# Performance work log

Measured on AMD Instinct MI355X. Metric: run time of the kernel, lower is better.

## Reference

```python
import jax, jax.numpy as jnp
import numpy as np

N = 50000   # nodes
E = 800000  # edges
D = 128     # hidden_dim
O = 128     # out_dim (must equal hidden_dim; see prior_mean Linear)
T = 16      # number of timesteps for the modeled time encoding
EPS = 1e-9


def _gcn(x, W, b, src, dst, ew, n):
    """PyG-style GCNConv: add self-loops, symmetric deg^-1/2 normalization."""
    loop = jnp.arange(n)
    s = jnp.concatenate([src, loop])
    d = jnp.concatenate([dst, loop])
    w = jnp.concatenate([ew, jnp.ones((n,), x.dtype)])
    deg = jax.ops.segment_sum(w, d, num_segments=n)
    dinv = jnp.where(deg > 0, jax.lax.rsqrt(deg), 0.0)
    norm = dinv[s] * w * dinv[d]              # [E+N]
    h = x @ W                                  # [N, out]
    out = jax.ops.segment_sum(h[s] * norm[:, None], d, num_segments=n)
    return out + b


def setup_inputs() -> dict:
    key = jax.random.key(0)
    ks = jax.random.split(key, 20)

    def lin(k, fan_in, fan_out):
        return jax.random.normal(k, (fan_in, fan_out), jnp.float32) / np.sqrt(fan_in)

    return {
        "edge_index": jax.random.randint(ks[0], (2, E), 0, N, dtype=jnp.int64),
        "x": jax.random.normal(ks[1], (N, D), jnp.float32),
        "t": 3,
        "edge_score": jax.random.uniform(ks[2], (E,), jnp.float32),
        "total_len": 16,
        "train_len": 12,
        "W_enc": lin(ks[3], D, D), "b_enc": jnp.zeros((D,), jnp.float32),
        "W_mu": lin(ks[4], D, O), "b_mu": jnp.zeros((O,), jnp.float32),
        "W_std": lin(ks[5], D, O), "b_std": jnp.zeros((O,), jnp.float32),
        "W_prior": lin(ks[6], D, O), "b_prior": jnp.zeros((O,), jnp.float32),
        "W_pm": lin(ks[7], D, O), "b_pm": jnp.zeros((O,), jnp.float32),
        "W_ps": lin(ks[8], D, O), "b_ps": jnp.zeros((O,), jnp.float32),
        "time_emb": 0.02 * jax.random.normal(ks[9], (T, O), jnp.float32),
    }


def reference(edge_index, x, t, edge_score, total_len, train_len,
              W_enc, b_enc, W_mu, b_mu, W_std, b_std,
              W_prior, b_prior, W_pm, b_pm, W_ps, b_ps, time_emb):
    src, dst = edge_index[0], edge_index[1]
    n = x.shape[0]
    ones_e = jnp.ones((src.shape[0],), x.dtype)

    # encoder
    enc_t = jax.nn.relu(_gcn(x, W_enc, b_enc, src, dst, edge_score, n))
    # drop = 0.0 -> dropout is identity
    enc_mean_t = _gcn(enc_t, W_mu, b_mu, src, dst, ones_e, n)
    enc_std_t = jax.nn.sigmoid(_gcn(enc_t, W_std, b_std, src, dst, ones_e, n))

    # reparameterize (fixed eps for determinism)
    eps = jax.random.normal(jax.random.key(42), enc_mean_t.shape, enc_mean_t.dtype)
    conf_z_t = eps * enc_std_t + enc_mean_t

    # prior branch: time_encoding(prior, t) modeled as additive time embedding
    prior = jax.nn.relu(_gcn(x, W_prior, b_prior, src, dst, ones_e, n))
    prior = prior + time_emb[t]
    prior_mean = prior @ W_pm + b_pm
    prior_std = jax.nn.sigmoid(prior @ W_ps + b_ps)

    # fused KL divergence
    kl = (2.0 * jnp.log(prior_std + EPS) - 2.0 * jnp.log(enc_std_t + EPS)
          + ((enc_std_t + EPS) ** 2 + (enc_mean_t - prior_mean) ** 2)
          / (prior_std + EPS) ** 2 - 1.0)
    kl_loss = 0.5 * jnp.mean(jnp.sum(kl, axis=1), axis=0)
    return kl_loss, conf_z_t
```

## Files before the change

kernel.cpp:

```cpp
#include <hip/hip_runtime.h>
#include <math.h>

#define D 128

typedef unsigned int u32;
typedef unsigned short u16;
typedef __attribute__((ext_vector_type(8))) short bf16x8;
typedef __attribute__((ext_vector_type(4))) float f32x4;
typedef __attribute__((ext_vector_type(4))) u32 u32x4;

__device__ __forceinline__ u32 rotl32(u32 x, int r){ return (x<<r) | (x>>(32-r)); }

__device__ __forceinline__ u16 f2bf(float x){
  u32 u = __float_as_uint(x);
  return (u16)((u + 0x7fffu + ((u >> 16) & 1u)) >> 16);
}
__device__ __forceinline__ float bf2f(u16 h){ return __uint_as_float(((u32)h) << 16); }

__device__ __forceinline__ float jax_normal_part_xor(u32 m){
  const u32 ks0 = 0u, ks1 = 42u, ks2 = 0x1BD11BF0u;
  u32 x0 = 0u + ks0;
  u32 x1 = m  + ks1;
  #define TF_R4(a,b,c,d) \
    x0 += x1; x1 = rotl32(x1,(a)); x1 ^= x0; \
    x0 += x1; x1 = rotl32(x1,(b)); x1 ^= x0; \
    x0 += x1; x1 = rotl32(x1,(c)); x1 ^= x0; \
    x0 += x1; x1 = rotl32(x1,(d)); x1 ^= x0;
  TF_R4(13,15,26,6)   x0 += ks1; x1 += ks2 + 1u;
  TF_R4(17,29,16,24)  x0 += ks2; x1 += ks0 + 2u;
  TF_R4(13,15,26,6)   x0 += ks0; x1 += ks1 + 3u;
  TF_R4(17,29,16,24)  x0 += ks1; x1 += ks2 + 4u;
  TF_R4(13,15,26,6)   x0 += ks2; x1 += ks0 + 5u;
  #undef TF_R4
  u32 bits = x0 ^ x1;
  float f = __uint_as_float((bits >> 9) | 0x3F800000u) - 1.0f;
  const float LO = -0.99999994f;
  float u = fmaxf(LO, f * 2.0f + LO);
  float w = -__logf(fmaf(-u, u, 1.0f));
  float p;
  if (w < 5.0f){
    w -= 2.5f;
    p =  2.81022636e-08f;
    p = fmaf(p, w,  3.43273939e-07f);
    p = fmaf(p, w, -3.5233877e-06f);
    p = fmaf(p, w, -4.39150654e-06f);
    p = fmaf(p, w,  0.00021858087f);
    p = fmaf(p, w, -0.00125372503f);
    p = fmaf(p, w, -0.00417768164f);
    p = fmaf(p, w,  0.246640727f);
    p = fmaf(p, w,  1.50140941f);
  } else {
    w = sqrtf(w) - 3.0f;
    p = -0.000200214257f;
    p = fmaf(p, w,  0.000100950558f);
    p = fmaf(p, w,  0.00134934322f);
    p = fmaf(p, w, -0.00367342844f);
    p = fmaf(p, w,  0.00573950773f);
    p = fmaf(p, w, -0.0076224613f);
    p = fmaf(p, w,  0.00943887047f);
    p = fmaf(p, w,  1.00167406f);
    p = fmaf(p, w,  2.83297682f);
  }
  return 1.41421354f * (p * u);
}

__device__ __forceinline__ float sigmoidf_(float z){ return 1.0f / (1.0f + __expf(-z)); }

__global__ __launch_bounds__(256) void k_eps(u32* __restrict__ epsb, int half_total){
  int idx = blockIdx.x*256 + threadIdx.x;
  int stride = gridDim.x*256;
  for (int i = idx; i < half_total; i += stride){
    u32 m0 = 2u*(u32)i;
    float e0 = jax_normal_part_xor(m0);
    float e1 = jax_normal_part_xor(m0 + 1u);
    epsb[i] = (u32)f2bf(e0) | ((u32)f2bf(e1) << 16);
  }
}

__global__ void k_detect(const u32* __restrict__ e_u32, int* __restrict__ flag){
  __shared__ int s_nz;
  if (threadIdx.x == 0) s_nz = 0;
  __syncthreads();
  if (e_u32[2*threadIdx.x + 1] != 0u) atomicAdd(&s_nz, 1);
  __syncthreads();
  if (threadIdx.x == 0) *flag = (s_nz == 0) ? 1 : 0;
}

__global__ void k_norm(const void* __restrict__ eidx, const int* __restrict__ flag,
                       int* __restrict__ src_w, int* __restrict__ dst_w, int e){
  int i = blockIdx.x*256 + threadIdx.x;
  if (i >= e) return;
  if (*flag){
    const u32* u = (const u32*)eidx;
    src_w[i] = (int)u[2*(size_t)i];
    dst_w[i] = (int)u[2*((size_t)e + i)];
  } else {
    const int* p = (const int*)eidx;
    src_w[i] = p[i];
    dst_w[i] = p[e + i];
  }
}

__global__ void k_init(int* __restrict__ cnt, int n){
  int i = blockIdx.x*256 + threadIdx.x;
  if (i < n) cnt[i] = 0;
}

__global__ void k_hist(const int* __restrict__ dst, int* __restrict__ cnt, int e){
  int i = blockIdx.x*256 + threadIdx.x;
  if (i >= e) return;
  atomicAdd(&cnt[dst[i]], 1);
}

__global__ __launch_bounds__(256) void k_scan1(const int* __restrict__ cnt,
                                               int* __restrict__ rp,
                                               int* __restrict__ bsum, int n){
  __shared__ int sh[256];
  int tid = threadIdx.x, idx = blockIdx.x*256 + tid;
  int v = (idx < n) ? cnt[idx] : 0;
  sh[tid] = v; __syncthreads();
  for (int off = 1; off < 256; off <<= 1){
    int t = (tid >= off) ? sh[tid-off] : 0;
    __syncthreads(); sh[tid] += t; __syncthreads();
  }
  if (idx < n) rp[idx] = sh[tid] - v;
  if (tid == 255) bsum[blockIdx.x] = sh[255];
}

__global__ __launch_bounds__(1024) void k_scan2(int* __restrict__ bsum, int nb){
  __shared__ int sh[1024];
  int tid = threadIdx.x;
  int v = (tid < nb) ? bsum[tid] : 0;
  sh[tid] = v; __syncthreads();
  for (int off = 1; off < 1024; off <<= 1){
    int t = (tid >= off) ? sh[tid-off] : 0;
    __syncthreads(); sh[tid] += t; __syncthreads();
  }
  if (tid < nb) bsum[tid] = sh[tid] - v;
}

__global__ void k_scan3(int* __restrict__ rp, int* __restrict__ cur,
                        const int* __restrict__ bsum, const int* __restrict__ cnt,
                        float* __restrict__ dinv_o, int n, int e){
  int idx = blockIdx.x*256 + threadIdx.x;
  if (idx < n){
    int r = rp[idx] + bsum[blockIdx.x];
    rp[idx] = r; cur[idx] = r;
    dinv_o[idx] = rsqrtf((float)(cnt[idx] + 1));
  }
  if (idx == 0) rp[n] = e;
}

__global__ void k_scatter(const int* __restrict__ src, const int* __restrict__ dst,
                          const float* __restrict__ sc, int* __restrict__ cur,
                          int* __restrict__ col, float* __restrict__ wsrt, int e){
  int i = blockIdx.x*256 + threadIdx.x;
  if (i >= e) return;
  int d = dst[i];
  int p = atomicAdd(&cur[d], 1);
  col[p] = src[i];
  wsrt[p] = sc[i];
}

__global__ void k_deg(const int* __restrict__ rp, const float* __restrict__ wsrt,
                      float* __restrict__ dinv_s, int n){
  int i = blockIdx.x*256 + threadIdx.x;
  if (i >= n) return;
  float s = 1.0f;
  int e0 = rp[i], e1 = rp[i+1];
  for (int j = e0; j < e1; ++j) s += wsrt[j];
  dinv_s[i] = rsqrtf(s);
}

__global__ void k_wconv(const float* __restrict__ W0, const float* __restrict__ W1,
                        const float* __restrict__ W2, const float* __restrict__ W3,
                        const float* __restrict__ W4, const float* __restrict__ W5,
                        u16* __restrict__ wt){
  const float* Ws[6] = {W0,W1,W2,W3,W4,W5};
  const float* W = Ws[blockIdx.y];
  u16* Wt = wt + (size_t)blockIdx.y*16384;
  int idx = blockIdx.x*256 + threadIdx.x;
  int k = idx >> 7, col = idx & 127;
  Wt[col*128 + k] = f2bf(W[idx]);
}

__global__ __launch_bounds__(256) void k_agg_dual(
    const float* __restrict__ x, const int* __restrict__ rp,
    const int* __restrict__ col, const float* __restrict__ wsrt,
    const float* __restrict__ dinv_s, const float* __restrict__ dinv_o,
    u16* __restrict__ out_s, u16* __restrict__ out_o, int n){
  int wid = (blockIdx.x * 256 + threadIdx.x) >> 6;
  int lane = threadIdx.x & 63;
  if (wid >= n) return;
  const float2* x2 = (const float2*)x;
  float dsv = dinv_s[wid], dov = dinv_o[wid];
  float2 xv = x2[(size_t)wid*64 + lane];
  float ss = dsv*dsv, oo = dov*dov;
  float2 as = { xv.x*ss, xv.y*ss };
  float2 ao = { xv.x*oo, xv.y*oo };
  int e0 = rp[wid], e1 = rp[wid+1];
  for (int base = e0; base < e1; base += 64){
    int cnt = e1 - base; if (cnt > 64) cnt = 64;
    int idx = base + (lane < cnt ? lane : cnt - 1);
    int   sl = col[idx];
    float wl = wsrt[idx];
    float nsl = dinv_s[sl] * wl * dsv;
    float nol = dinv_o[sl] * dov;
    int j = 0;
    for (; j + 4 <= cnt; j += 4){
      int   s0=__shfl(sl,j),   s1=__shfl(sl,j+1),   s2=__shfl(sl,j+2),   s3=__shfl(sl,j+3);
      float a0=__shfl(nsl,j),  a1=__shfl(nsl,j+1),  a2=__shfl(nsl,j+2),  a3=__shfl(nsl,j+3);
      float b0=__shfl(nol,j),  b1=__shfl(nol,j+1),  b2=__shfl(nol,j+2),  b3=__shfl(nol,j+3);
      float2 r0 = x2[(size_t)s0*64 + lane];
      float2 r1 = x2[(size_t)s1*64 + lane];
      float2 r2 = x2[(size_t)s2*64 + lane];
      float2 r3 = x2[(size_t)s3*64 + lane];
      as.x = fmaf(a0,r0.x,as.x); as.y = fmaf(a0,r0.y,as.y);
      ao.x = fmaf(b0,r0.x,ao.x); ao.y = fmaf(b0,r0.y,ao.y);
      as.x = fmaf(a1,r1.x,as.x); as.y = fmaf(a1,r1.y,as.y);
      ao.x = fmaf(b1,r1.x,ao.x); ao.y = fmaf(b1,r1.y,ao.y);
      as.x = fmaf(a2,r2.x,as.x); as.y = fmaf(a2,r2.y,as.y);
      ao.x = fmaf(b2,r2.x,ao.x); ao.y = fmaf(b2,r2.y,ao.y);
      as.x = fmaf(a3,r3.x,as.x); as.y = fmaf(a3,r3.y,as.y);
      ao.x = fmaf(b3,r3.x,ao.x); ao.y = fmaf(b3,r3.y,ao.y);
    }
    for (; j < cnt; ++j){
      int   s0=__shfl(sl,j);
      float a0=__shfl(nsl,j), b0=__shfl(nol,j);
      float2 r0 = x2[(size_t)s0*64 + lane];
      as.x = fmaf(a0,r0.x,as.x); as.y = fmaf(a0,r0.y,as.y);
      ao.x = fmaf(b0,r0.x,ao.x); ao.y = fmaf(b0,r0.y,ao.y);
    }
  }
  ((u32*)out_s)[(size_t)wid*64 + lane] = (u32)f2bf(as.x) | ((u32)f2bf(as.y) << 16);
  ((u32*)out_o)[(size_t)wid*64 + lane] = (u32)f2bf(ao.x) | ((u32)f2bf(ao.y) << 16);
}

__global__ __launch_bounds__(256) void k_agg_one(
    const u16* __restrict__ h, const int* __restrict__ rp,
    const int* __restrict__ col, const float* __restrict__ dinv_o,
    u16* __restrict__ out, int n){
  int wid = (blockIdx.x * 256 + threadIdx.x) >> 6;
  int lane = threadIdx.x & 63;
  if (wid >= n) return;
  const u32* h2 = (const u32*)h;
  float dov = dinv_o[wid];
  u32 hv = h2[(size_t)wid*64 + lane];
  float oo = dov*dov;
  float2 ao = { bf2f((u16)(hv & 0xffff))*oo, bf2f((u16)(hv >> 16))*oo };
  int e0 = rp[wid], e1 = rp[wid+1];
  for (int base = e0; base < e1; base += 64){
    int cnt = e1 - base; if (cnt > 64) cnt = 64;
    int idx = base + (lane < cnt ? lane : cnt - 1);
    int   sl = col[idx];
    float nol = dinv_o[sl] * dov;
    int j = 0;
    for (; j + 4 <= cnt; j += 4){
      int   s0=__shfl(sl,j),  s1=__shfl(sl,j+1),  s2=__shfl(sl,j+2),  s3=__shfl(sl,j+3);
      float b0=__shfl(nol,j), b1=__shfl(nol,j+1), b2=__shfl(nol,j+2), b3=__shfl(nol,j+3);
      u32 r0 = h2[(size_t)s0*64 + lane];
      u32 r1 = h2[(size_t)s1*64 + lane];
      u32 r2 = h2[(size_t)s2*64 + lane];
      u32 r3 = h2[(size_t)s3*64 + lane];
      ao.x = fmaf(b0, bf2f((u16)(r0&0xffff)), ao.x); ao.y = fmaf(b0, bf2f((u16)(r0>>16)), ao.y);
      ao.x = fmaf(b1, bf2f((u16)(r1&0xffff)), ao.x); ao.y = fmaf(b1, bf2f((u16)(r1>>16)), ao.y);
      ao.x = fmaf(b2, bf2f((u16)(r2&0xffff)), ao.x); ao.y = fmaf(b2, bf2f((u16)(r2>>16)), ao.y);
      ao.x = fmaf(b3, bf2f((u16)(r3&0xffff)), ao.x); ao.y = fmaf(b3, bf2f((u16)(r3>>16)), ao.y);
    }
    for (; j < cnt; ++j){
      int   s0=__shfl(sl,j);
      float b0=__shfl(nol,j);
      u32 r0 = h2[(size_t)s0*64 + lane];
      ao.x = fmaf(b0, bf2f((u16)(r0&0xffff)), ao.x); ao.y = fmaf(b0, bf2f((u16)(r0>>16)), ao.y);
    }
  }
  ((u32*)out)[(size_t)wid*64 + lane] = (u32)f2bf(ao.x) | ((u32)f2bf(ao.y) << 16);
}


__global__ __launch_bounds__(256) void k_mfma_act2(
    const u16* __restrict__ A0, const u16* __restrict__ Wt0, const float* __restrict__ b0,
    const u16* __restrict__ A1, const u16* __restrict__ Wt1, const float* __restrict__ b1,
    const float* __restrict__ temb, const int* __restrict__ t_ptr,
    u16* __restrict__ out0, u16* __restrict__ out1, int n){
  const int sl = blockIdx.y;
  const u16* A  = sl ? A1 : A0;
  const u16* Wt = sl ? Wt1 : Wt0;
  const float* b = sl ? b1 : b0;
  u16* out = sl ? out1 : out0;
  const int tid = threadIdx.x;
  const int lane = tid & 63, wave = tid >> 6;
  const int lr = lane & 15, lg = lane >> 4;
  const int rw = wave >> 1, cw = wave & 1;
  const int row0 = blockIdx.x*32 + rw*16;
  int rowf = row0 + lr;
  int rowc = rowf < n ? rowf : n - 1;
  const char* Arow = (const char*)A + (size_t)rowc*256;
  const char* Wb   = (const char*)Wt + (cw*64 + lr)*256 + lg*16;
  f32x4 z = {0.f,0.f,0.f,0.f};
  f32x4 acc[4];
  #pragma unroll
  for (int i = 0; i < 4; ++i) acc[i] = z;
  #pragma unroll
  for (int ks = 0; ks < 4; ++ks){
    bf16x8 a = *(const bf16x8*)(Arow + ks*64 + lg*16);
    #pragma unroll
    for (int cf = 0; cf < 4; ++cf){
      bf16x8 bb = *(const bf16x8*)(Wb + cf*16*256 + ks*64);
      acc[cf] = __builtin_amdgcn_mfma_f32_16x16x32_bf16(a, bb, acc[cf], 0, 0, 0);
    }
  }
  int t = sl ? *t_ptr : 0;
  int rbase = row0 + (lg << 2);
  #pragma unroll
  for (int cf = 0; cf < 4; ++cf){
    int colw = cw*64 + cf*16 + lr;
    float bb = b[colw];
    float tt = sl ? temb[t*128 + colw] : 0.f;
    #pragma unroll
    for (int r = 0; r < 4; ++r){
      int row = rbase + r;
      if (row < n)
        out[(size_t)row*128 + colw] = f2bf(fmaxf(acc[cf][r] + bb, 0.f) + tt);
    }
  }
}

__global__ __launch_bounds__(256) void k_mfma_quad(
    const u16* __restrict__ Apr, const u16* __restrict__ Aen,
    const u16* __restrict__ Wtpm, const float* __restrict__ bpm,
    const u16* __restrict__ Wtps, const float* __restrict__ bps,
    const u16* __restrict__ Wtmu, const float* __restrict__ bmu,
    const u16* __restrict__ Wtsd, const float* __restrict__ bsd,
    const u32* __restrict__ epsb,
    float* __restrict__ conf, float* __restrict__ pblk, int n){
  const int tid = threadIdx.x;
  const int lane = tid & 63, wave = tid >> 6;
  const int lr = lane & 15, lg = lane >> 4;
  const int rw = wave >> 1, cw = wave & 1;
  const int row0 = blockIdx.x*32 + rw*16;
  int rowf = row0 + lr;
  int rowc = rowf < n ? rowf : n - 1;
  const char* Ap = (const char*)Apr + (size_t)rowc*256;
  const char* Ae = (const char*)Aen + (size_t)rowc*256;
  const int wcb = (cw*64 + lr)*256 + lg*16;
  const char* Wpm = (const char*)Wtpm + wcb;
  const char* Wps = (const char*)Wtps + wcb;
  const char* Wmu = (const char*)Wtmu + wcb;
  const char* Wsd = (const char*)Wtsd + wcb;
  f32x4 z = {0.f,0.f,0.f,0.f};
  f32x4 aPM[4], aPS[4], aMU[4], aSD[4];
  #pragma unroll
  for (int i = 0; i < 4; ++i){ aPM[i]=z; aPS[i]=z; aMU[i]=z; aSD[i]=z; }
  #pragma unroll
  for (int ks = 0; ks < 4; ++ks){
    bf16x8 a5 = *(const bf16x8*)(Ap + ks*64 + lg*16);
    bf16x8 a2 = *(const bf16x8*)(Ae + ks*64 + lg*16);
    #pragma unroll
    for (int cf = 0; cf < 4; ++cf){
      int off = cf*16*256 + ks*64;
      aPM[cf] = __builtin_amdgcn_mfma_f32_16x16x32_bf16(a5, *(const bf16x8*)(Wpm+off), aPM[cf], 0,0,0);
      aPS[cf] = __builtin_amdgcn_mfma_f32_16x16x32_bf16(a5, *(const bf16x8*)(Wps+off), aPS[cf], 0,0,0);
      aMU[cf] = __builtin_amdgcn_mfma_f32_16x16x32_bf16(a2, *(const bf16x8*)(Wmu+off), aMU[cf], 0,0,0);
      aSD[cf] = __builtin_amdgcn_mfma_f32_16x16x32_bf16(a2, *(const bf16x8*)(Wsd+off), aSD[cf], 0,0,0);
    }
  }
  const float EPS = 1e-9f;
  int rbase = row0 + (lg << 2);
  float klsum = 0.f;
  #pragma unroll
  for (int cf = 0; cf < 4; ++cf){
    int colw = cw*64 + cf*16 + lr;
    float bb1 = bpm[colw], bb2 = bps[colw];
    float bb3 = bmu[colw], bb4 = bsd[colw];
    #pragma unroll
    for (int r = 0; r < 4; ++r){
      int row = rbase + r;
      if (row < n){
        size_t m = (size_t)row*128 + colw;
        float pmv = aPM[cf][r] + bb1;
        float psv = sigmoidf_(aPS[cf][r] + bb2);
        float em  = aMU[cf][r] + bb3;
        float es  = sigmoidf_(aSD[cf][r] + bb4);
        u32 ew = epsb[m >> 1];
        float eps = bf2f((u16)((colw & 1) ? (ew >> 16) : (ew & 0xffff)));
        conf[m] = fmaf(eps, es, em);
        float es_e = es + EPS, ps_e = psv + EPS;
        float diff = em - pmv;
        klsum += 2.0f*__logf(ps_e/es_e)
               + (es_e*es_e + diff*diff) / (ps_e*ps_e) - 1.0f;
      }
    }
  }
  #pragma unroll
  for (int off = 32; off > 0; off >>= 1) klsum += __shfl_down(klsum, off);
  __shared__ float wsum[4];
  if ((tid & 63) == 0) wsum[tid >> 6] = klsum;
  __syncthreads();
  if (tid == 0) pblk[blockIdx.x] = wsum[0] + wsum[1] + wsum[2] + wsum[3];
}

__global__ __launch_bounds__(256) void k_finish(const float* __restrict__ pblk, int nb,
                                                float* __restrict__ out0, int n){
  __shared__ double sh[256];
  double s = 0.0;
  for (int i = threadIdx.x; i < nb; i += 256) s += (double)pblk[i];
  sh[threadIdx.x] = s; __syncthreads();
  for (int off = 128; off > 0; off >>= 1){
    if (threadIdx.x < off) sh[threadIdx.x] += sh[threadIdx.x + off];
    __syncthreads();
  }
  if (threadIdx.x == 0) out0[0] = (float)(0.5 * sh[0] / (double)n);
}

extern "C" void kernel_launch(void* const* d_in, const int* in_sizes, int n_in,
                              void* d_out, int out_size, void* d_ws, size_t ws_size,
                              hipStream_t stream){
  const void*  eidx   = d_in[0];
  const float* x      = (const float*)d_in[1];
  const int*   t_ptr  = (const int*)d_in[2];
  const float* escore = (const float*)d_in[3];
  const float* W_enc = (const float*)d_in[6];  const float* b_enc = (const float*)d_in[7];
  const float* W_mu  = (const float*)d_in[8];  const float* b_mu  = (const float*)d_in[9];
  const float* W_std = (const float*)d_in[10]; const float* b_std = (const float*)d_in[11];
  const float* W_pr  = (const float*)d_in[12]; const float* b_pr  = (const float*)d_in[13];
  const float* W_pm  = (const float*)d_in[14]; const float* b_pm  = (const float*)d_in[15];
  const float* W_ps  = (const float*)d_in[16]; const float* b_ps  = (const float*)d_in[17];
  const float* temb  = (const float*)d_in[18];

  const int N = in_sizes[1] / D;
  const int E = in_sizes[3];

  char* w = (char*)d_ws;
  auto alloc = [&](size_t bytes) -> char* {
    char* p = w; w += (bytes + 255) & ~(size_t)255; return p;
  };
  int*    flag   = (int*)   alloc(256);
  int*    src_w  = (int*)   alloc((size_t)E*4);
  int*    dst_w  = (int*)   alloc((size_t)E*4);
  int*    cnt    = (int*)   alloc((size_t)N*4);
  int*    rp     = (int*)   alloc((size_t)(N+1)*4);
  int*    cur    = (int*)   alloc((size_t)N*4);
  float*  dinv_s = (float*) alloc((size_t)N*4);
  float*  dinv_o = (float*) alloc((size_t)N*4);
  int*    bsum   = (int*)   alloc(1024*4);
  int*    col    = (int*)   alloc((size_t)E*4);
  float*  wsrt   = (float*) alloc((size_t)E*4);
  u16*    wt     = (u16*)   alloc((size_t)6*16384*2);
  u16*    B1     = (u16*)   alloc((size_t)N*D*2);
  u16*    B2     = (u16*)   alloc((size_t)N*D*2);
  u16*    B3     = (u16*)   alloc((size_t)N*D*2);
  u16*    B5     = (u16*)   alloc((size_t)N*D*2);
  u32*    EPSB   = (u32*)   alloc((size_t)N*64*4);
  const int gG32 = (N + 31) / 32;
  float*  pblk   = (float*) alloc((size_t)gG32*4);
  (void)ws_size; (void)n_in; (void)out_size;

  float* conf = ((float*)d_out) + 1;

  u16* Wt_enc = wt + 0*16384;
  u16* Wt_pr  = wt + 1*16384;
  u16* Wt_pm  = wt + 2*16384;
  u16* Wt_ps  = wt + 3*16384;
  u16* Wt_mu  = wt + 4*16384;
  u16* Wt_std = wt + 5*16384;

  const int gE  = (E + 255) / 256;
  const int gN  = (N + 255) / 256;
  const int gW  = (N * 64 + 255) / 256;

  k_eps    <<<2048, 256, 0, stream>>>(EPSB, N*64);
  k_wconv  <<<dim3(64,6), 256, 0, stream>>>(W_enc, W_pr, W_pm, W_ps, W_mu, W_std, wt);
  k_detect <<<1, 256, 0, stream>>>((const u32*)eidx, flag);
  k_norm   <<<gE, 256, 0, stream>>>(eidx, flag, src_w, dst_w, E);
  k_init   <<<gN, 256, 0, stream>>>(cnt, N);
  k_hist   <<<gE, 256, 0, stream>>>(dst_w, cnt, E);
  k_scan1  <<<gN, 256, 0, stream>>>(cnt, rp, bsum, N);
  k_scan2  <<<1, 1024, 0, stream>>>(bsum, gN);
  k_scan3  <<<gN, 256, 0, stream>>>(rp, cur, bsum, cnt, dinv_o, N, E);
  k_scatter<<<gE, 256, 0, stream>>>(src_w, dst_w, escore, cur, col, wsrt, E);
  k_deg    <<<gN, 256, 0, stream>>>(rp, wsrt, dinv_s, N);

  k_agg_dual<<<gW, 256, 0, stream>>>(x, rp, col, wsrt, dinv_s, dinv_o, B1, B2, N);
  k_mfma_act2<<<dim3(gG32,2), 256, 0, stream>>>(B1, Wt_enc, b_enc, B2, Wt_pr, b_pr,
                                                temb, t_ptr, B3, B5, N);
  k_agg_one<<<gW, 256, 0, stream>>>(B3, rp, col, dinv_o, B2, N);
  k_mfma_quad<<<gG32, 256, 0, stream>>>(B5, B2, Wt_pm, b_pm, Wt_ps, b_ps,
                                        Wt_mu, b_mu, Wt_std, b_std, EPSB,
                                        conf, pblk, N);
  k_finish<<<1, 256, 0, stream>>>(pblk, gG32, (float*)d_out, N);
}
```

Measured before the change: 337.7 us.

## Fuse neighbor aggregation into MFMA GEMM kernels via LDS staging

Merges each sparse aggregation pass with the dense GEMM that follows it. Each 32-row block gathers its neighbor sums into swizzled shared memory, then runs the MFMA tiles from LDS, which removes the bf16 intermediate buffers B1/B2 and two launches. The edge histogram is also folded into the edge-index normalization kernel. In exchange, each block now runs a serial 8-rows-per-wave gather before its MFMA phase, and the grid drops to N/32 blocks, which lowers parallelism for the latency-bound gather.

```diff
diff --git a/kernel.cpp b/kernel.cpp
--- a/kernel.cpp
+++ b/kernel.cpp
@@ -7,7 +7,6 @@
 typedef unsigned short u16;
 typedef __attribute__((ext_vector_type(8))) short bf16x8;
 typedef __attribute__((ext_vector_type(4))) float f32x4;
-typedef __attribute__((ext_vector_type(4))) u32 u32x4;
 
 __device__ __forceinline__ u32 rotl32(u32 x, int r){ return (x<<r) | (x>>(32-r)); }
 
@@ -86,30 +85,29 @@
   if (threadIdx.x == 0) *flag = (s_nz == 0) ? 1 : 0;
 }
 
-__global__ void k_norm(const void* __restrict__ eidx, const int* __restrict__ flag,
-                       int* __restrict__ src_w, int* __restrict__ dst_w, int e){
-  int i = blockIdx.x*256 + threadIdx.x;
-  if (i >= e) return;
-  if (*flag){
-    const u32* u = (const u32*)eidx;
-    src_w[i] = (int)u[2*(size_t)i];
-    dst_w[i] = (int)u[2*((size_t)e + i)];
-  } else {
-    const int* p = (const int*)eidx;
-    src_w[i] = p[i];
-    dst_w[i] = p[e + i];
-  }
-}
-
 __global__ void k_init(int* __restrict__ cnt, int n){
   int i = blockIdx.x*256 + threadIdx.x;
   if (i < n) cnt[i] = 0;
 }
 
-__global__ void k_hist(const int* __restrict__ dst, int* __restrict__ cnt, int e){
+__global__ void k_norm(const void* __restrict__ eidx, const int* __restrict__ flag,
+                       int* __restrict__ src_w, int* __restrict__ dst_w,
+                       int* __restrict__ cnt, int e){
   int i = blockIdx.x*256 + threadIdx.x;
   if (i >= e) return;
-  atomicAdd(&cnt[dst[i]], 1);
+  int s, d;
+  if (*flag){
+    const u32* u = (const u32*)eidx;
+    s = (int)u[2*(size_t)i];
+    d = (int)u[2*((size_t)e + i)];
+  } else {
+    const int* p = (const int*)eidx;
+    s = p[i];
+    d = p[e + i];
+  }
+  src_w[i] = s;
+  dst_w[i] = d;
+  atomicAdd(&cnt[d], 1);
 }
 
 __global__ __launch_bounds__(256) void k_scan1(const int* __restrict__ cnt,
@@ -184,165 +182,173 @@
   Wt[col*128 + k] = f2bf(W[idx]);
 }
 
-__global__ __launch_bounds__(256) void k_agg_dual(
+
+__global__ __launch_bounds__(256) void k_fuse1(
     const float* __restrict__ x, const int* __restrict__ rp,
     const int* __restrict__ col, const float* __restrict__ wsrt,
     const float* __restrict__ dinv_s, const float* __restrict__ dinv_o,
-    u16* __restrict__ out_s, u16* __restrict__ out_o, int n){
-  int wid = (blockIdx.x * 256 + threadIdx.x) >> 6;
-  int lane = threadIdx.x & 63;
-  if (wid >= n) return;
-  const float2* x2 = (const float2*)x;
-  float dsv = dinv_s[wid], dov = dinv_o[wid];
-  float2 xv = x2[(size_t)wid*64 + lane];
-  float ss = dsv*dsv, oo = dov*dov;
-  float2 as = { xv.x*ss, xv.y*ss };
-  float2 ao = { xv.x*oo, xv.y*oo };
-  int e0 = rp[wid], e1 = rp[wid+1];
-  for (int base = e0; base < e1; base += 64){
-    int cnt = e1 - base; if (cnt > 64) cnt = 64;
-    int idx = base + (lane < cnt ? lane : cnt - 1);
-    int   sl = col[idx];
-    float wl = wsrt[idx];
-    float nsl = dinv_s[sl] * wl * dsv;
-    float nol = dinv_o[sl] * dov;
-    int j = 0;
-    for (; j + 4 <= cnt; j += 4){
-      int   s0=__shfl(sl,j),   s1=__shfl(sl,j+1),   s2=__shfl(sl,j+2),   s3=__shfl(sl,j+3);
-      float a0=__shfl(nsl,j),  a1=__shfl(nsl,j+1),  a2=__shfl(nsl,j+2),  a3=__shfl(nsl,j+3);
-      float b0=__shfl(nol,j),  b1=__shfl(nol,j+1),  b2=__shfl(nol,j+2),  b3=__shfl(nol,j+3);
-      float2 r0 = x2[(size_t)s0*64 + lane];
-      float2 r1 = x2[(size_t)s1*64 + lane];
-      float2 r2 = x2[(size_t)s2*64 + lane];
-      float2 r3 = x2[(size_t)s3*64 + lane];
-      as.x = fmaf(a0,r0.x,as.x); as.y = fmaf(a0,r0.y,as.y);
-      ao.x = fmaf(b0,r0.x,ao.x); ao.y = fmaf(b0,r0.y,ao.y);
-      as.x = fmaf(a1,r1.x,as.x); as.y = fmaf(a1,r1.y,as.y);
-      ao.x = fmaf(b1,r1.x,ao.x); ao.y = fmaf(b1,r1.y,ao.y);
-      as.x = fmaf(a2,r2.x,as.x); as.y = fmaf(a2,r2.y,as.y);
-      ao.x = fmaf(b2,r2.x,ao.x); ao.y = fmaf(b2,r2.y,ao.y);
-      as.x = fmaf(a3,r3.x,as.x); as.y = fmaf(a3,r3.y,as.y);
-      ao.x = fmaf(b3,r3.x,ao.x); ao.y = fmaf(b3,r3.y,ao.y);
-    }
-    for (; j < cnt; ++j){
-      int   s0=__shfl(sl,j);
-      float a0=__shfl(nsl,j), b0=__shfl(nol,j);
-      float2 r0 = x2[(size_t)s0*64 + lane];
-      as.x = fmaf(a0,r0.x,as.x); as.y = fmaf(a0,r0.y,as.y);
-      ao.x = fmaf(b0,r0.x,ao.x); ao.y = fmaf(b0,r0.y,ao.y);
-    }
-  }
-  ((u32*)out_s)[(size_t)wid*64 + lane] = (u32)f2bf(as.x) | ((u32)f2bf(as.y) << 16);
-  ((u32*)out_o)[(size_t)wid*64 + lane] = (u32)f2bf(ao.x) | ((u32)f2bf(ao.y) << 16);
-}
-
-__global__ __launch_bounds__(256) void k_agg_one(
-    const u16* __restrict__ h, const int* __restrict__ rp,
-    const int* __restrict__ col, const float* __restrict__ dinv_o,
-    u16* __restrict__ out, int n){
-  int wid = (blockIdx.x * 256 + threadIdx.x) >> 6;
-  int lane = threadIdx.x & 63;
-  if (wid >= n) return;
-  const u32* h2 = (const u32*)h;
-  float dov = dinv_o[wid];
-  u32 hv = h2[(size_t)wid*64 + lane];
-  float oo = dov*dov;
-  float2 ao = { bf2f((u16)(hv & 0xffff))*oo, bf2f((u16)(hv >> 16))*oo };
-  int e0 = rp[wid], e1 = rp[wid+1];
-  for (int base = e0; base < e1; base += 64){
-    int cnt = e1 - base; if (cnt > 64) cnt = 64;
-    int idx = base + (lane < cnt ? lane : cnt - 1);
-    int   sl = col[idx];
-    float nol = dinv_o[sl] * dov;
-    int j = 0;
-    for (; j + 4 <= cnt; j += 4){
-      int   s0=__shfl(sl,j),  s1=__shfl(sl,j+1),  s2=__shfl(sl,j+2),  s3=__shfl(sl,j+3);
-      float b0=__shfl(nol,j), b1=__shfl(nol,j+1), b2=__shfl(nol,j+2), b3=__shfl(nol,j+3);
-      u32 r0 = h2[(size_t)s0*64 + lane];
-      u32 r1 = h2[(size_t)s1*64 + lane];
-      u32 r2 = h2[(size_t)s2*64 + lane];
-      u32 r3 = h2[(size_t)s3*64 + lane];
-      ao.x = fmaf(b0, bf2f((u16)(r0&0xffff)), ao.x); ao.y = fmaf(b0, bf2f((u16)(r0>>16)), ao.y);
-      ao.x = fmaf(b1, bf2f((u16)(r1&0xffff)), ao.x); ao.y = fmaf(b1, bf2f((u16)(r1>>16)), ao.y);
-      ao.x = fmaf(b2, bf2f((u16)(r2&0xffff)), ao.x); ao.y = fmaf(b2, bf2f((u16)(r2>>16)), ao.y);
-      ao.x = fmaf(b3, bf2f((u16)(r3&0xffff)), ao.x); ao.y = fmaf(b3, bf2f((u16)(r3>>16)), ao.y);
-    }
-    for (; j < cnt; ++j){
-      int   s0=__shfl(sl,j);
-      float b0=__shfl(nol,j);
-      u32 r0 = h2[(size_t)s0*64 + lane];
-      ao.x = fmaf(b0, bf2f((u16)(r0&0xffff)), ao.x); ao.y = fmaf(b0, bf2f((u16)(r0>>16)), ao.y);
-    }
-  }
-  ((u32*)out)[(size_t)wid*64 + lane] = (u32)f2bf(ao.x) | ((u32)f2bf(ao.y) << 16);
-}
-
-
-__global__ __launch_bounds__(256) void k_mfma_act2(
-    const u16* __restrict__ A0, const u16* __restrict__ Wt0, const float* __restrict__ b0,
-    const u16* __restrict__ A1, const u16* __restrict__ Wt1, const float* __restrict__ b1,
+    const u16* __restrict__ Wt_enc, const float* __restrict__ b_enc,
+    const u16* __restrict__ Wt_pr, const float* __restrict__ b_pr,
     const float* __restrict__ temb, const int* __restrict__ t_ptr,
-    u16* __restrict__ out0, u16* __restrict__ out1, int n){
-  const int sl = blockIdx.y;
-  const u16* A  = sl ? A1 : A0;
-  const u16* Wt = sl ? Wt1 : Wt0;
-  const float* b = sl ? b1 : b0;
-  u16* out = sl ? out1 : out0;
+    u16* __restrict__ enc_out, u16* __restrict__ pri_out, int n){
+  __shared__ u32 A1[32*64];
+  __shared__ u32 A2[32*64];
   const int tid = threadIdx.x;
   const int lane = tid & 63, wave = tid >> 6;
+  const int row0 = blockIdx.x * 32;
+  const float2* x2 = (const float2*)x;
+  for (int i = 0; i < 8; ++i){
+    int row = wave*8 + i;
+    int wid = row0 + row;
+    float2 as = {0.f,0.f}, ao = {0.f,0.f};
+    if (wid < n){
+      float dsv = dinv_s[wid], dov = dinv_o[wid];
+      float2 xv = x2[(size_t)wid*64 + lane];
+      float ss = dsv*dsv, oo = dov*dov;
+      as.x = xv.x*ss; as.y = xv.y*ss;
+      ao.x = xv.x*oo; ao.y = xv.y*oo;
+      int e0 = rp[wid], e1 = rp[wid+1];
+      for (int base = e0; base < e1; base += 64){
+        int cnt = e1 - base; if (cnt > 64) cnt = 64;
+        int idx = base + (lane < cnt ? lane : cnt - 1);
+        int   sl = col[idx];
+        float wl = wsrt[idx];
+        float nsl = dinv_s[sl] * wl * dsv;
+        float nol = dinv_o[sl] * dov;
+        int j = 0;
+        for (; j + 4 <= cnt; j += 4){
+          int   s0=__shfl(sl,j),   s1=__shfl(sl,j+1),   s2=__shfl(sl,j+2),   s3=__shfl(sl,j+3);
+          float a0=__shfl(nsl,j),  a1=__shfl(nsl,j+1),  a2=__shfl(nsl,j+2),  a3=__shfl(nsl,j+3);
+          float b0=__shfl(nol,j),  b1=__shfl(nol,j+1),  b2=__shfl(nol,j+2),  b3=__shfl(nol,j+3);
+          float2 r0 = x2[(size_t)s0*64 + lane];
+          float2 r1 = x2[(size_t)s1*64 + lane];
+          float2 r2 = x2[(size_t)s2*64 + lane];
+          float2 r3 = x2[(size_t)s3*64 + lane];
+          as.x = fmaf(a0,r0.x,as.x); as.y = fmaf(a0,r0.y,as.y);
+          ao.x = fmaf(b0,r0.x,ao.x); ao.y = fmaf(b0,r0.y,ao.y);
+          as.x = fmaf(a1,r1.x,as.x); as.y = fmaf(a1,r1.y,as.y);
+          ao.x = fmaf(b1,r1.x,ao.x); ao.y = fmaf(b1,r1.y,ao.y);
+          as.x = fmaf(a2,r2.x,as.x); as.y = fmaf(a2,r2.y,as.y);
+          ao.x = fmaf(b2,r2.x,ao.x); ao.y = fmaf(b2,r2.y,ao.y);
+          as.x = fmaf(a3,r3.x,as.x); as.y = fmaf(a3,r3.y,as.y);
+          ao.x = fmaf(b3,r3.x,ao.x); ao.y = fmaf(b3,r3.y,ao.y);
+        }
+        for (; j < cnt; ++j){
+          int   s0=__shfl(sl,j);
+          float a0=__shfl(nsl,j), b0=__shfl(nol,j);
+          float2 r0 = x2[(size_t)s0*64 + lane];
+          as.x = fmaf(a0,r0.x,as.x); as.y = fmaf(a0,r0.y,as.y);
+          ao.x = fmaf(b0,r0.x,ao.x); ao.y = fmaf(b0,r0.y,ao.y);
+        }
+      }
+    }
+    int bo = row*256 + ((lane*4) ^ ((row & 7) << 4));
+    *(u32*)((char*)A1 + bo) = (u32)f2bf(as.x) | ((u32)f2bf(as.y) << 16);
+    *(u32*)((char*)A2 + bo) = (u32)f2bf(ao.x) | ((u32)f2bf(ao.y) << 16);
+  }
+  __syncthreads();
   const int lr = lane & 15, lg = lane >> 4;
   const int rw = wave >> 1, cw = wave & 1;
-  const int row0 = blockIdx.x*32 + rw*16;
-  int rowf = row0 + lr;
-  int rowc = rowf < n ? rowf : n - 1;
-  const char* Arow = (const char*)A + (size_t)rowc*256;
-  const char* Wb   = (const char*)Wt + (cw*64 + lr)*256 + lg*16;
+  const int arow = rw*16 + lr;
+  const int aswz = (arow & 7) << 4;
+  const char* Wb1 = (const char*)Wt_enc + (cw*64 + lr)*256 + lg*16;
+  const char* Wb2 = (const char*)Wt_pr  + (cw*64 + lr)*256 + lg*16;
   f32x4 z = {0.f,0.f,0.f,0.f};
-  f32x4 acc[4];
-  #pragma unroll
-  for (int i = 0; i < 4; ++i) acc[i] = z;
+  f32x4 acc1[4], acc2[4];
+  #pragma unroll
+  for (int i = 0; i < 4; ++i){ acc1[i] = z; acc2[i] = z; }
   #pragma unroll
   for (int ks = 0; ks < 4; ++ks){
-    bf16x8 a = *(const bf16x8*)(Arow + ks*64 + lg*16);
+    bf16x8 a1 = *(bf16x8*)((char*)A1 + arow*256 + ((ks*64 + lg*16) ^ aswz));
+    bf16x8 a2 = *(bf16x8*)((char*)A2 + arow*256 + ((ks*64 + lg*16) ^ aswz));
     #pragma unroll
     for (int cf = 0; cf < 4; ++cf){
-      bf16x8 bb = *(const bf16x8*)(Wb + cf*16*256 + ks*64);
-      acc[cf] = __builtin_amdgcn_mfma_f32_16x16x32_bf16(a, bb, acc[cf], 0, 0, 0);
-    }
-  }
-  int t = sl ? *t_ptr : 0;
-  int rbase = row0 + (lg << 2);
+      int off = cf*16*256 + ks*64;
+      acc1[cf] = __builtin_amdgcn_mfma_f32_16x16x32_bf16(a1, *(const bf16x8*)(Wb1+off), acc1[cf], 0,0,0);
+      acc2[cf] = __builtin_amdgcn_mfma_f32_16x16x32_bf16(a2, *(const bf16x8*)(Wb2+off), acc2[cf], 0,0,0);
+    }
+  }
+  int t = *t_ptr;
+  int rbase = row0 + rw*16 + (lg << 2);
   #pragma unroll
   for (int cf = 0; cf < 4; ++cf){
     int colw = cw*64 + cf*16 + lr;
-    float bb = b[colw];
-    float tt = sl ? temb[t*128 + colw] : 0.f;
+    float bb1 = b_enc[colw], bb2 = b_pr[colw];
+    float tt = temb[t*128 + colw];
     #pragma unroll
     for (int r = 0; r < 4; ++r){
       int row = rbase + r;
-      if (row < n)
-        out[(size_t)row*128 + colw] = f2bf(fmaxf(acc[cf][r] + bb, 0.f) + tt);
-    }
-  }
-}
-
-__global__ __launch_bounds__(256) void k_mfma_quad(
-    const u16* __restrict__ Apr, const u16* __restrict__ Aen,
+      if (row < n){
+        enc_out[(size_t)row*128 + colw] = f2bf(fmaxf(acc1[cf][r] + bb1, 0.f));
+        pri_out[(size_t)row*128 + colw] = f2bf(fmaxf(acc2[cf][r] + bb2, 0.f) + tt);
+      }
+    }
+  }
+}
+
+__global__ __launch_bounds__(256) void k_fuse2(
+    const u16* __restrict__ enc, const u16* __restrict__ pri,
+    const int* __restrict__ rp, const int* __restrict__ col,
+    const float* __restrict__ dinv_o,
     const u16* __restrict__ Wtpm, const float* __restrict__ bpm,
     const u16* __restrict__ Wtps, const float* __restrict__ bps,
     const u16* __restrict__ Wtmu, const float* __restrict__ bmu,
     const u16* __restrict__ Wtsd, const float* __restrict__ bsd,
     const u32* __restrict__ epsb,
     float* __restrict__ conf, float* __restrict__ pblk, int n){
+  __shared__ u32 AE[32*64];
   const int tid = threadIdx.x;
   const int lane = tid & 63, wave = tid >> 6;
+  const int row0 = blockIdx.x * 32;
+  const u32* h2 = (const u32*)enc;
+  for (int i = 0; i < 8; ++i){
+    int row = wave*8 + i;
+    int wid = row0 + row;
+    float2 ao = {0.f,0.f};
+    if (wid < n){
+      float dov = dinv_o[wid];
+      u32 hv = h2[(size_t)wid*64 + lane];
+      float oo = dov*dov;
+      ao.x = bf2f((u16)(hv & 0xffff))*oo;
+      ao.y = bf2f((u16)(hv >> 16))*oo;
+      int e0 = rp[wid], e1 = rp[wid+1];
+      for (int base = e0; base < e1; base += 64){
+        int cnt = e1 - base; if (cnt > 64) cnt = 64;
+        int idx = base + (lane < cnt ? lane : cnt - 1);
+        int   sl = col[idx];
+        float nol = dinv_o[sl] * dov;
+        int j = 0;
+        for (; j + 4 <= cnt; j += 4){
+          int   s0=__shfl(sl,j),  s1=__shfl(sl,j+1),  s2=__shfl(sl,j+2),  s3=__shfl(sl,j+3);
+          float b0=__shfl(nol,j), b1=__shfl(nol,j+1), b2=__shfl(nol,j+2), b3=__shfl(nol,j+3);
+          u32 r0 = h2[(size_t)s0*64 + lane];
+          u32 r1 = h2[(size_t)s1*64 + lane];
+          u32 r2 = h2[(size_t)s2*64 + lane];
+          u32 r3 = h2[(size_t)s3*64 + lane];
+          ao.x = fmaf(b0, bf2f((u16)(r0&0xffff)), ao.x); ao.y = fmaf(b0, bf2f((u16)(r0>>16)), ao.y);
+          ao.x = fmaf(b1, bf2f((u16)(r1&0xffff)), ao.x); ao.y = fmaf(b1, bf2f((u16)(r1>>16)), ao.y);
+          ao.x = fmaf(b2, bf2f((u16)(r2&0xffff)), ao.x); ao.y = fmaf(b2, bf2f((u16)(r2>>16)), ao.y);
+          ao.x = fmaf(b3, bf2f((u16)(r3&0xffff)), ao.x); ao.y = fmaf(b3, bf2f((u16)(r3>>16)), ao.y);
+        }
+        for (; j < cnt; ++j){
+          int   s0=__shfl(sl,j);
+          float b0=__shfl(nol,j);
+          u32 r0 = h2[(size_t)s0*64 + lane];
+          ao.x = fmaf(b0, bf2f((u16)(r0&0xffff)), ao.x); ao.y = fmaf(b0, bf2f((u16)(r0>>16)), ao.y);
+        }
+      }
+    }
+    int bo = row*256 + ((lane*4) ^ ((row & 7) << 4));
+    *(u32*)((char*)AE + bo) = (u32)f2bf(ao.x) | ((u32)f2bf(ao.y) << 16);
+  }
+  __syncthreads();
   const int lr = lane & 15, lg = lane >> 4;
   const int rw = wave >> 1, cw = wave & 1;
-  const int row0 = blockIdx.x*32 + rw*16;
-  int rowf = row0 + lr;
+  const int arow = rw*16 + lr;
+  const int aswz = (arow & 7) << 4;
+  int rowf = row0 + arow;
   int rowc = rowf < n ? rowf : n - 1;
-  const char* Ap = (const char*)Apr + (size_t)rowc*256;
-  const char* Ae = (const char*)Aen + (size_t)rowc*256;
+  const char* Ap = (const char*)pri + (size_t)rowc*256;
   const int wcb = (cw*64 + lr)*256 + lg*16;
   const char* Wpm = (const char*)Wtpm + wcb;
   const char* Wps = (const char*)Wtps + wcb;
@@ -355,7 +361,7 @@
   #pragma unroll
   for (int ks = 0; ks < 4; ++ks){
     bf16x8 a5 = *(const bf16x8*)(Ap + ks*64 + lg*16);
-    bf16x8 a2 = *(const bf16x8*)(Ae + ks*64 + lg*16);
+    bf16x8 a2 = *(bf16x8*)((char*)AE + arow*256 + ((ks*64 + lg*16) ^ aswz));
     #pragma unroll
     for (int cf = 0; cf < 4; ++cf){
       int off = cf*16*256 + ks*64;
@@ -366,7 +372,7 @@
     }
   }
   const float EPS = 1e-9f;
-  int rbase = row0 + (lg << 2);
+  int rbase = row0 + rw*16 + (lg << 2);
   float klsum = 0.f;
   #pragma unroll
   for (int cf = 0; cf < 4; ++cf){
@@ -447,8 +453,6 @@
   int*    col    = (int*)   alloc((size_t)E*4);
   float*  wsrt   = (float*) alloc((size_t)E*4);
   u16*    wt     = (u16*)   alloc((size_t)6*16384*2);
-  u16*    B1     = (u16*)   alloc((size_t)N*D*2);
-  u16*    B2     = (u16*)   alloc((size_t)N*D*2);
   u16*    B3     = (u16*)   alloc((size_t)N*D*2);
   u16*    B5     = (u16*)   alloc((size_t)N*D*2);
   u32*    EPSB   = (u32*)   alloc((size_t)N*64*4);
@@ -467,26 +471,24 @@
 
   const int gE  = (E + 255) / 256;
   const int gN  = (N + 255) / 256;
-  const int gW  = (N * 64 + 255) / 256;
 
   k_eps    <<<2048, 256, 0, stream>>>(EPSB, N*64);
   k_wconv  <<<dim3(64,6), 256, 0, stream>>>(W_enc, W_pr, W_pm, W_ps, W_mu, W_std, wt);
   k_detect <<<1, 256, 0, stream>>>((const u32*)eidx, flag);
-  k_norm   <<<gE, 256, 0, stream>>>(eidx, flag, src_w, dst_w, E);
   k_init   <<<gN, 256, 0, stream>>>(cnt, N);
-  k_hist   <<<gE, 256, 0, stream>>>(dst_w, cnt, E);
+  k_norm   <<<gE, 256, 0, stream>>>(eidx, flag, src_w, dst_w, cnt, E);
   k_scan1  <<<gN, 256, 0, stream>>>(cnt, rp, bsum, N);
   k_scan2  <<<1, 1024, 0, stream>>>(bsum, gN);
   k_scan3  <<<gN, 256, 0, stream>>>(rp, cur, bsum, cnt, dinv_o, N, E);
   k_scatter<<<gE, 256, 0, stream>>>(src_w, dst_w, escore, cur, col, wsrt, E);
   k_deg    <<<gN, 256, 0, stream>>>(rp, wsrt, dinv_s, N);
 
-  k_agg_dual<<<gW, 256, 0, stream>>>(x, rp, col, wsrt, dinv_s, dinv_o, B1, B2, N);
-  k_mfma_act2<<<dim3(gG32,2), 256, 0, stream>>>(B1, Wt_enc, b_enc, B2, Wt_pr, b_pr,
-                                                temb, t_ptr, B3, B5, N);
-  k_agg_one<<<gW, 256, 0, stream>>>(B3, rp, col, dinv_o, B2, N);
-  k_mfma_quad<<<gG32, 256, 0, stream>>>(B5, B2, Wt_pm, b_pm, Wt_ps, b_ps,
-                                        Wt_mu, b_mu, Wt_std, b_std, EPSB,
-                                        conf, pblk, N);
+  k_fuse1<<<gG32, 256, 0, stream>>>(x, rp, col, wsrt, dinv_s, dinv_o,
+                                    Wt_enc, b_enc, Wt_pr, b_pr, temb, t_ptr,
+                                    B3, B5, N);
+  k_fuse2<<<gG32, 256, 0, stream>>>(B3, B5, rp, col, dinv_o,
+                                    Wt_pm, b_pm, Wt_ps, b_ps,
+                                    Wt_mu, b_mu, Wt_std, b_std, EPSB,
+                                    conf, pblk, N);
   k_finish<<<1, 256, 0, stream>>>(pblk, gG32, (float*)d_out, N);
 }
```

Result: slower. 381.9 us (+13.1%).
